# Kernel optimization log

Measured on AMD Instinct MI355X. Metric: run time of the kernel, lower is better.

## Reference

```python
import jax, jax.numpy as jnp
import numpy as np

NODE_DIM, HID, NCLS = 16, 64, 2
B, T, N = 16, 64, 400


def setup_inputs() -> dict:
    key = jax.random.key(0)
    ks = jax.random.split(key, 10)
    s = lambda k, shape: jax.random.normal(k, shape, dtype=jnp.float32) * 0.05
    return {
        "x_seq": jax.random.normal(ks[0], (B, T, N, NODE_DIM), dtype=jnp.float32),
        "adj_seq": jax.random.uniform(ks[1], (B, T, N, N), dtype=jnp.float32),
        "Wp": s(ks[2], (NODE_DIM, HID)),
        "bp": s(ks[3], (HID,)),
        "W_ih": s(ks[4], (3 * HID, HID)),
        "W_hh": s(ks[5], (3 * HID, HID)),
        "b_ih": s(ks[6], (3 * HID,)),
        "b_hh": s(ks[7], (3 * HID,)),
        "Wc": s(ks[8], (HID, NCLS)),
        "bc": s(ks[9], (NCLS,)),
    }


def _gru_last(feats, W_ih, W_hh, b_ih, b_hh):
    # feats: [B, T, H] -> final hidden state [B, H] (torch nn.GRU equations)
    H = W_hh.shape[1]

    def step(h, x_t):
        gi = x_t @ W_ih.T + b_ih            # [B, 3H]
        gh = h @ W_hh.T + b_hh              # [B, 3H]
        i_r, i_z, i_n = gi[:, :H], gi[:, H:2 * H], gi[:, 2 * H:]
        h_r, h_z, h_n = gh[:, :H], gh[:, H:2 * H], gh[:, 2 * H:]
        r = jax.nn.sigmoid(i_r + h_r)
        z = jax.nn.sigmoid(i_z + h_z)
        n = jnp.tanh(i_n + r * h_n)
        h_new = (1.0 - z) * n + z * h
        return h_new, None

    h0 = jnp.zeros((feats.shape[0], H), dtype=feats.dtype)
    h_last, _ = jax.lax.scan(step, h0, jnp.swapaxes(feats, 0, 1))  # scan over T
    return h_last


def reference(x_seq, adj_seq, Wp, bp, W_ih, W_hh, b_ih, b_hh, Wc, bc):
    n_nodes = x_seq.shape[2]
    # node projection for all (b, t) at once: [B, T, N, H]
    h = jnp.einsum('btnd,dh->btnh', x_seq, Wp) + bp
    # adjacency aggregation + mean pool over nodes, fused: mean_n (adj @ h)
    feats = jnp.einsum('btnm,btmh->bth', adj_seq, h) / n_nodes  # [B, T, H]
    z = _gru_last(feats, W_ih, W_hh, b_ih, b_hh)                 # [B, H]
    logits = z @ Wc + bc                                         # [B, NCLS]
    return logits
```

## Files before the change

### kernel.cpp

```cpp
#include <hip/hip_runtime.h>

#define NDIM 16
#define HID  64
#define G3   192
#define NCLS 2
#define BB   16
#define TT   64
#define NN   400

typedef float v4f __attribute__((ext_vector_type(4)));

__global__ __launch_bounds__(512, 8) void feats_gi_kernel(
    const float* __restrict__ x_seq,
    const float* __restrict__ adj_seq,
    const float* __restrict__ Wp,
    const float* __restrict__ bp,
    const float* __restrict__ W_ih,
    const float* __restrict__ b_ih,
    float* __restrict__ gi_out)
{
    const int bt  = blockIdx.x;
    const int tid = threadIdx.x;
    const float* __restrict__ xbt = x_seq + (size_t)bt * NN * NDIM;

    __shared__ v4f   cpart[5][100];
    __shared__ __align__(16) float colsum[NN];
    __shared__ float wred[8][17];
    __shared__ float yf[17];
    __shared__ float ffin[HID];

    if (tid < 500) {
        const v4f* __restrict__ base =
            reinterpret_cast<const v4f*>(adj_seq + (size_t)bt * NN * NN) + tid;
        v4f cs = (v4f)(0.f);
        #pragma unroll 8
        for (int k = 0; k < 80; k++) {
            v4f v = __builtin_nontemporal_load(base + 500 * k);
            cs += v;
        }
        cpart[tid / 100][tid % 100] = cs;
    }
    __syncthreads();
    if (tid < 100) {
        v4f s = ((cpart[0][tid] + cpart[1][tid]) +
                 (cpart[2][tid] + cpart[3][tid])) + cpart[4][tid];
        *reinterpret_cast<v4f*>(colsum + 4 * tid) = s;
    }
    __syncthreads();

    float y[17];
    #pragma unroll
    for (int i = 0; i < 17; i++) y[i] = 0.f;
    if (tid < NN) {
        const int m = tid;
        float c = colsum[m];
        y[16] = c;
        const float4* xp = reinterpret_cast<const float4*>(xbt + m * NDIM);
        float4 v0 = xp[0], v1 = xp[1], v2 = xp[2], v3 = xp[3];
        y[0]  = c * v0.x;  y[1]  = c * v0.y;  y[2]  = c * v0.z;  y[3]  = c * v0.w;
        y[4]  = c * v1.x;  y[5]  = c * v1.y;  y[6]  = c * v1.z;  y[7]  = c * v1.w;
        y[8]  = c * v2.x;  y[9]  = c * v2.y;  y[10] = c * v2.z;  y[11] = c * v2.w;
        y[12] = c * v3.x;  y[13] = c * v3.y;  y[14] = c * v3.z;  y[15] = c * v3.w;
    }
    #pragma unroll
    for (int off = 32; off >= 1; off >>= 1) {
        #pragma unroll
        for (int i = 0; i < 17; i++) y[i] += __shfl_down(y[i], off, 64);
    }
    const int lane = tid & 63;
    const int wv   = tid >> 6;
    if (lane == 0) {
        #pragma unroll
        for (int i = 0; i < 17; i++) wred[wv][i] = y[i];
    }
    __syncthreads();
    if (tid < 17) {
        float s = 0.f;
        #pragma unroll
        for (int w = 0; w < 8; w++) s += wred[w][tid];
        yf[tid] = s;
    }
    __syncthreads();

    if (tid < HID) {
        float acc = 0.f;
        #pragma unroll
        for (int d = 0; d < NDIM; d++) acc += yf[d] * Wp[d * HID + tid];
        ffin[tid] = (acc + yf[16] * bp[tid]) * (1.0f / (float)NN);
    }
    __syncthreads();

    if (tid < G3) {
        const float4* wr = reinterpret_cast<const float4*>(W_ih + tid * HID);
        float acc = b_ih[tid];
        #pragma unroll
        for (int k4 = 0; k4 < HID / 4; k4++) {
            float4 w = wr[k4];
            acc += ffin[4 * k4 + 0] * w.x + ffin[4 * k4 + 1] * w.y
                 + ffin[4 * k4 + 2] * w.z + ffin[4 * k4 + 3] * w.w;
        }
        gi_out[(size_t)bt * G3 + tid] = acc;
    }
}

__device__ __forceinline__ float fast_sigmoid(float x) {
    x = fminf(fmaxf(x, -20.f), 20.f);
    return __builtin_amdgcn_rcpf(1.f + __expf(-x));
}
__device__ __forceinline__ float fast_tanh(float x) {
    x = fminf(fmaxf(x, -10.f), 10.f);
    float e2 = __expf(2.f * x);
    return (e2 - 1.f) * __builtin_amdgcn_rcpf(e2 + 1.f);
}

__global__ __launch_bounds__(192) void gru_kernel(
    const float* __restrict__ gi_all,
    const float* __restrict__ W_hh,
    const float* __restrict__ b_hh,
    const float* __restrict__ Wc,
    const float* __restrict__ bc,
    float* __restrict__ out)
{
    const int b = blockIdx.x;
    const int j = threadIdx.x;

    float whh[HID];
    #pragma unroll
    for (int k4 = 0; k4 < HID / 4; k4++) {
        float4 w = *reinterpret_cast<const float4*>(W_hh + j * HID + 4 * k4);
        whh[4 * k4 + 0] = w.x; whh[4 * k4 + 1] = w.y;
        whh[4 * k4 + 2] = w.z; whh[4 * k4 + 3] = w.w;
    }
    const float bh = b_hh[j];

    __shared__ __align__(16) float hst[HID];
    __shared__ float rbuf[HID], zbuf[HID], inb[HID], hnb[HID];
    float hreg = 0.f;
    if (j < HID) hst[j] = 0.f;
    __syncthreads();

    const float* __restrict__ gi = gi_all + (size_t)b * TT * G3;
    float gcur = gi[j];

    for (int t = 0; t < TT; t++) {
        float gnext = (t + 1 < TT) ? gi[(t + 1) * G3 + j] : 0.f;

        float a0 = 0.f, a1 = 0.f, a2 = 0.f, a3 = 0.f;
        #pragma unroll
        for (int k4 = 0; k4 < HID / 4; k4 += 4) {
            float4 h0 = *reinterpret_cast<const float4*>(hst + 4 * (k4 + 0));
            float4 h1 = *reinterpret_cast<const float4*>(hst + 4 * (k4 + 1));
            float4 h2 = *reinterpret_cast<const float4*>(hst + 4 * (k4 + 2));
            float4 h3 = *reinterpret_cast<const float4*>(hst + 4 * (k4 + 3));
            a0 += h0.x*whh[4*k4+0]  + h0.y*whh[4*k4+1]  + h0.z*whh[4*k4+2]  + h0.w*whh[4*k4+3];
            a1 += h1.x*whh[4*k4+4]  + h1.y*whh[4*k4+5]  + h1.z*whh[4*k4+6]  + h1.w*whh[4*k4+7];
            a2 += h2.x*whh[4*k4+8]  + h2.y*whh[4*k4+9]  + h2.z*whh[4*k4+10] + h2.w*whh[4*k4+11];
            a3 += h3.x*whh[4*k4+12] + h3.y*whh[4*k4+13] + h3.z*whh[4*k4+14] + h3.w*whh[4*k4+15];
        }
        float gh = ((a0 + a1) + (a2 + a3)) + bh;

        if (j < 64) {
            rbuf[j] = fast_sigmoid(gcur + gh);
        } else if (j < 128) {
            zbuf[j - 64] = fast_sigmoid(gcur + gh);
        } else {
            inb[j - 128] = gcur;
            hnb[j - 128] = gh;
        }
        __syncthreads();

        if (j < HID) {
            float nv = fast_tanh(inb[j] + rbuf[j] * hnb[j]);
            float z  = zbuf[j];
            hreg = (1.f - z) * nv + z * hreg;
            hst[j] = hreg;
        }
        __syncthreads();
        gcur = gnext;
    }

    if (j < NCLS) {
        float acc = bc[j];
        #pragma unroll
        for (int h = 0; h < HID; h++) acc += hst[h] * Wc[h * NCLS + j];
        out[b * NCLS + j] = acc;
    }
}

extern "C" void kernel_launch(void* const* d_in, const int* in_sizes, int n_in,
                              void* d_out, int out_size, void* d_ws, size_t ws_size,
                              hipStream_t stream) {
    const float* x_seq   = (const float*)d_in[0];
    const float* adj_seq = (const float*)d_in[1];
    const float* Wp      = (const float*)d_in[2];
    const float* bp      = (const float*)d_in[3];
    const float* W_ih    = (const float*)d_in[4];
    const float* W_hh    = (const float*)d_in[5];
    const float* b_ih    = (const float*)d_in[6];
    const float* b_hh    = (const float*)d_in[7];
    const float* Wc      = (const float*)d_in[8];
    const float* bc      = (const float*)d_in[9];

    float* gi  = (float*)d_ws;
    float* out = (float*)d_out;

    feats_gi_kernel<<<BB * TT, 512, 0, stream>>>(x_seq, adj_seq, Wp, bp,
                                                 W_ih, b_ih, gi);
    gru_kernel<<<BB, 192, 0, stream>>>(gi, W_hh, b_hh, Wc, bc, out);
}
```

Measured before the change: 150.3 us.

## Split adjacency column-sum into separate kernel from projection and gate-input stage

Moves the bandwidth-heavy adjacency column summation into its own kernel that writes column sums to workspace, and lets a second kernel consume them for the projection and input-gate computation. The column-sum loop now uses two interleaved accumulators to shorten the dependency chain. The intent is to let the streaming kernel run lean with high occupancy while the lighter reduction work runs separately, at the cost of an extra launch and a small workspace round trip.

```diff
diff --git a/kernel.cpp b/kernel.cpp
--- a/kernel.cpp
+++ b/kernel.cpp
@@ -10,9 +10,39 @@
 
 typedef float v4f __attribute__((ext_vector_type(4)));
 
-__global__ __launch_bounds__(512, 8) void feats_gi_kernel(
+#define GI_OFS (2u << 20)
+
+__global__ __launch_bounds__(512, 8) void colsum_kernel(
+    const float* __restrict__ adj_seq,
+    float* __restrict__ colsum_out)
+{
+    const int bt  = blockIdx.x;
+    const int tid = threadIdx.x;
+
+    __shared__ v4f cpart[5][100];
+
+    if (tid < 500) {
+        const v4f* __restrict__ base =
+            reinterpret_cast<const v4f*>(adj_seq + (size_t)bt * NN * NN) + tid;
+        v4f cs0 = (v4f)(0.f), cs1 = (v4f)(0.f);
+        #pragma unroll 8
+        for (int k = 0; k < 80; k++) {
+            v4f v = __builtin_nontemporal_load(base + 500 * k);
+            if (k & 1) cs1 += v; else cs0 += v;
+        }
+        cpart[tid / 100][tid % 100] = cs0 + cs1;
+    }
+    __syncthreads();
+    if (tid < 100) {
+        v4f s = ((cpart[0][tid] + cpart[1][tid]) +
+                 (cpart[2][tid] + cpart[3][tid])) + cpart[4][tid];
+        reinterpret_cast<v4f*>(colsum_out)[(size_t)bt * 100 + tid] = s;
+    }
+}
+
+__global__ __launch_bounds__(512, 4) void reduce_kernel(
     const float* __restrict__ x_seq,
-    const float* __restrict__ adj_seq,
+    const float* __restrict__ colsum_in,
     const float* __restrict__ Wp,
     const float* __restrict__ bp,
     const float* __restrict__ W_ih,
@@ -23,28 +53,14 @@
     const int tid = threadIdx.x;
     const float* __restrict__ xbt = x_seq + (size_t)bt * NN * NDIM;
 
-    __shared__ v4f   cpart[5][100];
     __shared__ __align__(16) float colsum[NN];
     __shared__ float wred[8][17];
     __shared__ float yf[17];
     __shared__ float ffin[HID];
 
-    if (tid < 500) {
-        const v4f* __restrict__ base =
-            reinterpret_cast<const v4f*>(adj_seq + (size_t)bt * NN * NN) + tid;
-        v4f cs = (v4f)(0.f);
-        #pragma unroll 8
-        for (int k = 0; k < 80; k++) {
-            v4f v = __builtin_nontemporal_load(base + 500 * k);
-            cs += v;
-        }
-        cpart[tid / 100][tid % 100] = cs;
-    }
-    __syncthreads();
     if (tid < 100) {
-        v4f s = ((cpart[0][tid] + cpart[1][tid]) +
-                 (cpart[2][tid] + cpart[3][tid])) + cpart[4][tid];
-        *reinterpret_cast<v4f*>(colsum + 4 * tid) = s;
+        reinterpret_cast<v4f*>(colsum)[tid] =
+            reinterpret_cast<const v4f*>(colsum_in)[(size_t)bt * 100 + tid];
     }
     __syncthreads();
 
@@ -201,10 +217,12 @@
     const float* Wc      = (const float*)d_in[8];
     const float* bc      = (const float*)d_in[9];
 
-    float* gi  = (float*)d_ws;
-    float* out = (float*)d_out;
-
-    feats_gi_kernel<<<BB * TT, 512, 0, stream>>>(x_seq, adj_seq, Wp, bp,
-                                                 W_ih, b_ih, gi);
-    gru_kernel<<<BB, 192, 0, stream>>>(gi, W_hh, b_hh, Wc, bc, out);
-}
+    float* colsum = (float*)d_ws;
+    float* gi     = (float*)((char*)d_ws + GI_OFS);
+    float* outp   = (float*)d_out;
+
+    colsum_kernel<<<BB * TT, 512, 0, stream>>>(adj_seq, colsum);
+    reduce_kernel<<<BB * TT, 512, 0, stream>>>(x_seq, colsum, Wp, bp,
+                                               W_ih, b_ih, gi);
+    gru_kernel<<<BB, 192, 0, stream>>>(gi, W_hh, b_hh, Wc, bc, outp);
+}
```

Measured after the change: 156.2 us. 1.04x slower.
